# Kernel optimization log

Hardware: AMD Instinct MI355X
Metric: run time of the kernel (lower is better)

## Reference

```python
import jax, jax.numpy as jnp
import numpy as np

B, S, D = 1, 2048, 4096
H, KVH, HD = 32, 8, 128
WIN = 2048
REPEATS = H // KVH
SCALE = HD ** -0.5
NEG = -1e9


def setup_inputs() -> dict:
    key = jax.random.key(0)
    ks = jax.random.split(key, 5)
    x = jax.random.normal(ks[0], (B, S, D), dtype=jnp.float32) * 0.02
    wq = jax.random.normal(ks[1], (H * HD, D), dtype=jnp.float32) * (D ** -0.5)
    wk = jax.random.normal(ks[2], (KVH * HD, D), dtype=jnp.float32) * (D ** -0.5)
    wv = jax.random.normal(ks[3], (KVH * HD, D), dtype=jnp.float32) * (D ** -0.5)
    wo = jax.random.normal(ks[4], (H * HD, D), dtype=jnp.float32).T * ((H * HD) ** -0.5)
    wo = jnp.asarray(wo)  # [D, H*HD] torch-style (out, in) = (D, H*HD)
    positions = jnp.arange(S, dtype=jnp.int32)
    # rotary tables: freqs_cis[s, j] = exp(i * s * theta_j), theta_j = 10000^(-2j/HD)
    theta = 10000.0 ** (-jnp.arange(0, HD, 2, dtype=jnp.float32) / HD)  # [HD/2]
    ang = positions[:, None].astype(jnp.float32) * theta[None, :]       # [S, HD/2]
    freqs_cos = jnp.cos(ang)
    freqs_sin = jnp.sin(ang)
    # sliding-window causal additive mask [S, S]
    i = jnp.arange(S)[:, None]
    j = jnp.arange(S)[None, :]
    allowed = (j <= i) & (i - j < WIN)
    mask = jnp.where(allowed, 0.0, NEG).astype(jnp.float32)
    return {"x": x, "freqs_cos": freqs_cos, "freqs_sin": freqs_sin,
            "wq": wq, "wk": wk, "wv": wv, "wo": wo,
            "mask": mask, "positions": positions}


def _apply_rope(t, cos, sin):
    # t: [B, S, h, HD]; pairs are (even, odd) interleaved -> complex mul
    tr = t[..., 0::2]  # real parts [B,S,h,HD/2]
    ti = t[..., 1::2]  # imag parts
    c = cos[None, :, None, :]
    s = sin[None, :, None, :]
    out_r = tr * c - ti * s
    out_i = tr * s + ti * c
    return jnp.stack([out_r, out_i], axis=-1).reshape(t.shape)


def reference(x, freqs_cos, freqs_sin, wq, wk, wv, wo, mask, positions):
    bsz, seqlen, _ = x.shape
    q = (x @ wq.T).reshape(bsz, seqlen, H, HD)
    k = (x @ wk.T).reshape(bsz, seqlen, KVH, HD)
    v = (x @ wv.T).reshape(bsz, seqlen, KVH, HD)
    q = _apply_rope(q, freqs_cos, freqs_sin)
    k = _apply_rope(k, freqs_cos, freqs_sin)
    # GQA: repeat_interleave kv heads to match query heads (prefill path)
    k = jnp.repeat(k, REPEATS, axis=2)  # [B,S,H,HD]
    v = jnp.repeat(v, REPEATS, axis=2)
    scores = jnp.einsum("bqhd,bkhd->bhqk", q, k) * SCALE
    scores = scores + mask[None, None, :, :]
    probs = jax.nn.softmax(scores, axis=-1)
    out = jnp.einsum("bhqk,bkhd->bqhd", probs, v)
    out = out.reshape(bsz, seqlen, H * HD)
    return out @ wo.T
```

## Files before the change

kernel.cpp:

```cpp
#include <hip/hip_runtime.h>
#include <hip/hip_bf16.h>
#include <stdint.h>

#define SEQ    2048
#define DMODEL 4096
#define NH     32
#define NKVH   8
#define HDIM   128
#define KVD    (NKVH*HDIM)
#define QD     (NH*HDIM)
#define QKVN   (QD + 2*KVD)
#define ASCALE 0.08838834764831845f

typedef __attribute__((ext_vector_type(8))) short s8v;
typedef __attribute__((ext_vector_type(4))) short s4v;
typedef __attribute__((ext_vector_type(4))) float f4v;

#define MFMA16(acc, a, b) \
  asm("v_mfma_f32_16x16x32_bf16 %0, %1, %2, %0" : "+v"(acc) : "v"(a), "v"(b))

#define SBAR() do { __builtin_amdgcn_sched_barrier(0); \
                    __builtin_amdgcn_s_barrier();      \
                    __builtin_amdgcn_sched_barrier(0); } while (0)

__device__ __forceinline__ void gl2lds16(const void* g, void* l) {
  __builtin_amdgcn_global_load_lds(
      (const __attribute__((address_space(1))) void*)g,
      (__attribute__((address_space(3))) void*)l, 16, 0, 0);
}

__global__ __launch_bounds__(256) void k_cvt5(const float* __restrict__ x,
                                              const float* __restrict__ wq,
                                              const float* __restrict__ wk,
                                              const float* __restrict__ wv,
                                              const float* __restrict__ wo,
                                              __hip_bfloat16* __restrict__ xb,
                                              __hip_bfloat16* __restrict__ wf,
                                              __hip_bfloat16* __restrict__ wob) {
  int i = blockIdx.x * 256 + threadIdx.x;
  const float* src;
  __hip_bfloat16* dst;
  float scale = 1.0f;
  if (i < 1048576)       { src = x;  dst = xb; }
  else if (i < 3145728)  { src = wq; dst = wf;  i -= 1048576; scale = ASCALE; }
  else if (i < 3670016)  { src = wk; dst = wf + (size_t)QD * DMODEL;  i -= 3145728; }
  else if (i < 4194304)  { src = wv; dst = wf + (size_t)(QD + KVD) * DMODEL; i -= 3670016; }
  else                   { src = wo; dst = wob; i -= 4194304; }
  const float4* p = (const float4*)src + (size_t)i * 2;
  float4 a = p[0], b = p[1];
  union { __hip_bfloat16 h[8]; s8v v; } o;
  o.h[0] = __float2bfloat16(a.x * scale); o.h[1] = __float2bfloat16(a.y * scale);
  o.h[2] = __float2bfloat16(a.z * scale); o.h[3] = __float2bfloat16(a.w * scale);
  o.h[4] = __float2bfloat16(b.x * scale); o.h[5] = __float2bfloat16(b.y * scale);
  o.h[6] = __float2bfloat16(b.z * scale); o.h[7] = __float2bfloat16(b.w * scale);
  *(s8v*)(dst + (size_t)i * 8) = o.v;
}

__global__ __launch_bounds__(256) void k_rope(__hip_bfloat16* __restrict__ t,
                                              const float* __restrict__ fc,
                                              const float* __restrict__ fs, int heads) {
  int pid = blockIdx.x * 256 + threadIdx.x;
  int i = pid & 63;
  int rest = pid >> 6;
  int h = rest % heads;
  int s = rest / heads;
  size_t base = ((size_t)s * heads + h) * HDIM + 2 * i;
  uint32_t u = *(const uint32_t*)(t + base);
  __hip_bfloat16 hh[2]; *(uint32_t*)hh = u;
  float tr = __bfloat162float(hh[0]), ti = __bfloat162float(hh[1]);
  float c = fc[(size_t)s * 64 + i], sv = fs[(size_t)s * 64 + i];
  hh[0] = __float2bfloat16(tr * c - ti * sv);
  hh[1] = __float2bfloat16(tr * sv + ti * c);
  *(uint32_t*)(t + base) = *(uint32_t*)hh;
}

__global__ __launch_bounds__(512, 2) void k_qkv(const __hip_bfloat16* __restrict__ A,
                                                const __hip_bfloat16* __restrict__ W,
                                                __hip_bfloat16* __restrict__ Qb,
                                                __hip_bfloat16* __restrict__ Kc,
                                                __hip_bfloat16* __restrict__ Vt) {
  __shared__ __align__(16) __hip_bfloat16 sm[2][256 * 64 + 192 * 64];
  const int t5 = threadIdx.x;
  const int wave = t5 >> 6, lane = t5 & 63;
  const int lrow = lane & 15, kq = lane >> 4;
  const int wm = wave >> 1, wn = wave & 1;
  const int mt = blockIdx.x & 7, nt = blockIdx.x >> 3;
  const int m0 = mt * 256, n0 = nt * 192;

  auto stageA = [&](int p, int kt) {
#pragma unroll
    for (int it = 0; it < 4; ++it) {
      int chunk = it * 512 + t5;
      int r = chunk >> 3, cc = ((chunk & 7) ^ (r & 7)) * 8;
      gl2lds16(A + (size_t)(m0 + r) * DMODEL + kt * 64 + cc,
               (char*)&sm[p][0] + it * 8192 + wave * 1024);
    }
  };
  auto stageB = [&](int p, int kt) {
#pragma unroll
    for (int it = 0; it < 3; ++it) {
      int chunk = it * 512 + t5;
      int r = chunk >> 3, cc = ((chunk & 7) ^ (r & 7)) * 8;
      gl2lds16(W + (size_t)(n0 + r) * DMODEL + kt * 64 + cc,
               (char*)&sm[p][0] + 32768 + it * 8192 + wave * 1024);
    }
  };

  f4v acc[4][6] = {};

  stageA(0, 0); stageB(0, 0);
  stageA(1, 1); stageB(1, 1);

  const int NT = DMODEL / 64;
#pragma unroll 2
  for (int t = 0; t < NT; ++t) {
    const int p = t & 1;
    const __hip_bfloat16* As = &sm[p][0];
    const __hip_bfloat16* Bs = &sm[p][256 * 64];

    __builtin_amdgcn_sched_barrier(0);
    if (t == NT - 1) asm volatile("s_waitcnt vmcnt(0)" ::: "memory");
    else             asm volatile("s_waitcnt vmcnt(7)" ::: "memory");
    __builtin_amdgcn_s_barrier();
    __builtin_amdgcn_sched_barrier(0);

    s8v a0[4], b0[6];
#pragma unroll
    for (int m = 0; m < 4; ++m) {
      int row = wm * 64 + m * 16 + lrow;
      a0[m] = *(const s8v*)&As[row * 64 + ((kq * 8) ^ ((row & 7) << 3))];
    }
#pragma unroll
    for (int n = 0; n < 6; ++n) {
      int row = wn * 96 + n * 16 + lrow;
      b0[n] = *(const s8v*)&Bs[row * 64 + ((kq * 8) ^ ((row & 7) << 3))];
    }
    __builtin_amdgcn_s_setprio(1);
#pragma unroll
    for (int m = 0; m < 2; ++m)
#pragma unroll
      for (int n = 0; n < 6; ++n) MFMA16(acc[m][n], a0[m], b0[n]);
    __builtin_amdgcn_s_setprio(0);
    SBAR();

    s8v a1[4], b1[6];
#pragma unroll
    for (int m = 0; m < 4; ++m) {
      int row = wm * 64 + m * 16 + lrow;
      a1[m] = *(const s8v*)&As[row * 64 + ((32 + kq * 8) ^ ((row & 7) << 3))];
    }
#pragma unroll
    for (int n = 0; n < 6; ++n) {
      int row = wn * 96 + n * 16 + lrow;
      b1[n] = *(const s8v*)&Bs[row * 64 + ((32 + kq * 8) ^ ((row & 7) << 3))];
    }
    __builtin_amdgcn_s_setprio(1);
#pragma unroll
    for (int m = 2; m < 4; ++m)
#pragma unroll
      for (int n = 0; n < 6; ++n) MFMA16(acc[m][n], a0[m], b0[n]);
    __builtin_amdgcn_s_setprio(0);
    SBAR();

    if (t + 2 < NT) stageA(p, t + 2);
    __builtin_amdgcn_s_setprio(1);
#pragma unroll
    for (int m = 0; m < 2; ++m)
#pragma unroll
      for (int n = 0; n < 6; ++n) MFMA16(acc[m][n], a1[m], b1[n]);
    __builtin_amdgcn_s_setprio(0);
    SBAR();

    if (t + 2 < NT) stageB(p, t + 2);
    __builtin_amdgcn_s_setprio(1);
#pragma unroll
    for (int m = 2; m < 4; ++m)
#pragma unroll
      for (int n = 0; n < 6; ++n) MFMA16(acc[m][n], a1[m], b1[n]);
    __builtin_amdgcn_s_setprio(0);
  }

#pragma unroll
  for (int m = 0; m < 4; ++m)
#pragma unroll
    for (int n = 0; n < 6; ++n) {
      int c = n0 + wn * 96 + n * 16 + lrow;
      int r0 = m0 + wm * 64 + m * 16 + kq * 4;
      if (c < QD) {
#pragma unroll
        for (int j = 0; j < 4; ++j)
          Qb[(size_t)(r0 + j) * QD + c] = __float2bfloat16(acc[m][n][j]);
      } else if (c < QD + KVD) {
#pragma unroll
        for (int j = 0; j < 4; ++j)
          Kc[(size_t)(r0 + j) * KVD + (c - QD)] = __float2bfloat16(acc[m][n][j]);
      } else {
        union { __hip_bfloat16 b[4]; s4v v; } u;
#pragma unroll
        for (int j = 0; j < 4; ++j) u.b[j] = __float2bfloat16(acc[m][n][j]);
        *(s4v*)&Vt[(size_t)(c - QD - KVD) * SEQ + r0] = u.v;
      }
    }
}

__global__ __launch_bounds__(512, 2) void k_oproj(const __hip_bfloat16* __restrict__ A,
                                                  const __hip_bfloat16* __restrict__ B,
                                                  float* __restrict__ C) {
  __shared__ __align__(16) __hip_bfloat16 sm[2][128 * 64 + 256 * 64];
  const int t5 = threadIdx.x;
  const int wave = t5 >> 6, lane = t5 & 63;
  const int lrow = lane & 15, kq = lane >> 4;
  const int wm = wave >> 2, wn = wave & 3;
  const int m0 = blockIdx.y * 128, n0 = blockIdx.x * 256;

  auto stageA = [&](int p, int kt) {
#pragma unroll
    for (int it = 0; it < 2; ++it) {
      int chunk = it * 512 + t5;
      int r = chunk >> 3, cc = ((chunk & 7) ^ (r & 7)) * 8;
      gl2lds16(A + (size_t)(m0 + r) * QD + kt * 64 + cc,
               (char*)&sm[p][0] + it * 8192 + wave * 1024);
    }
  };
  auto stageB = [&](int p, int kt) {
#pragma unroll
    for (int it = 0; it < 4; ++it) {
      int chunk = it * 512 + t5;
      int r = chunk >> 3, cc = ((chunk & 7) ^ (r & 7)) * 8;
      gl2lds16(B + (size_t)(n0 + r) * QD + kt * 64 + cc,
               (char*)&sm[p][0] + 16384 + it * 8192 + wave * 1024);
    }
  };

  f4v acc[4][4] = {};

  stageA(0, 0); stageB(0, 0);
  stageA(1, 1); stageB(1, 1);

  const int NT = QD / 64;
#pragma unroll 2
  for (int t = 0; t < NT; ++t) {
    const int p = t & 1;
    const __hip_bfloat16* As = &sm[p][0];
    const __hip_bfloat16* Bs = &sm[p][128 * 64];

    __builtin_amdgcn_sched_barrier(0);
    if (t == NT - 1) asm volatile("s_waitcnt vmcnt(0)" ::: "memory");
    else             asm volatile("s_waitcnt vmcnt(6)" ::: "memory");
    __builtin_amdgcn_s_barrier();
    __builtin_amdgcn_sched_barrier(0);

    s8v a0[4], b0[4];
#pragma unroll
    for (int m = 0; m < 4; ++m) {
      int row = wm * 64 + m * 16 + lrow;
      a0[m] = *(const s8v*)&As[row * 64 + ((kq * 8) ^ ((row & 7) << 3))];
    }
#pragma unroll
    for (int n = 0; n < 4; ++n) {
      int row = wn * 64 + n * 16 + lrow;
      b0[n] = *(const s8v*)&Bs[row * 64 + ((kq * 8) ^ ((row & 7) << 3))];
    }
    __builtin_amdgcn_s_setprio(1);
#pragma unroll
    for (int m = 0; m < 2; ++m)
#pragma unroll
      for (int n = 0; n < 4; ++n) MFMA16(acc[m][n], a0[m], b0[n]);
    __builtin_amdgcn_s_setprio(0);
    SBAR();

    s8v a1[4], b1[4];
#pragma unroll
    for (int m = 0; m < 4; ++m) {
      int row = wm * 64 + m * 16 + lrow;
      a1[m] = *(const s8v*)&As[row * 64 + ((32 + kq * 8) ^ ((row & 7) << 3))];
    }
#pragma unroll
    for (int n = 0; n < 4; ++n) {
      int row = wn * 64 + n * 16 + lrow;
      b1[n] = *(const s8v*)&Bs[row * 64 + ((32 + kq * 8) ^ ((row & 7) << 3))];
    }
    __builtin_amdgcn_s_setprio(1);
#pragma unroll
    for (int m = 2; m < 4; ++m)
#pragma unroll
      for (int n = 0; n < 4; ++n) MFMA16(acc[m][n], a0[m], b0[n]);
    __builtin_amdgcn_s_setprio(0);
    SBAR();

    if (t + 2 < NT) stageA(p, t + 2);
    __builtin_amdgcn_s_setprio(1);
#pragma unroll
    for (int m = 0; m < 2; ++m)
#pragma unroll
      for (int n = 0; n < 4; ++n) MFMA16(acc[m][n], a1[m], b1[n]);
    __builtin_amdgcn_s_setprio(0);
    SBAR();

    if (t + 2 < NT) stageB(p, t + 2);
    __builtin_amdgcn_s_setprio(1);
#pragma unroll
    for (int m = 2; m < 4; ++m)
#pragma unroll
      for (int n = 0; n < 4; ++n) MFMA16(acc[m][n], a1[m], b1[n]);
    __builtin_amdgcn_s_setprio(0);
  }

#pragma unroll
  for (int m = 0; m < 4; ++m)
#pragma unroll
    for (int n = 0; n < 4; ++n)
#pragma unroll
      for (int j = 0; j < 4; ++j) {
        int r = m0 + wm * 64 + m * 16 + kq * 4 + j;
        int c = n0 + wn * 64 + n * 16 + lrow;
        C[(size_t)r * DMODEL + c] = acc[m][n][j];
      }
}

__global__ __launch_bounds__(256, 2) void k_flash(const __hip_bfloat16* __restrict__ Q,
                                                  const __hip_bfloat16* __restrict__ Kb,
                                                  const __hip_bfloat16* __restrict__ Vtg,
                                                  __hip_bfloat16* __restrict__ O) {
  __shared__ __align__(16) __hip_bfloat16 Ks[2][64 * 128];
  __shared__ __align__(16) __hip_bfloat16 Vs[128 * 64];
  __shared__ __align__(16) __hip_bfloat16 Ps[4][16 * 64];
  const int qp = blockIdx.x, h = blockIdx.y, g = h >> 2;
  const int t = threadIdx.x, wave = t >> 6, lane = t & 63;
  const int lrow = lane & 15, kq = lane >> 4;
  const int qtA = qp, qtB = 31 - qp;

  s8v qfA[4], qfB[4];
  {
    const int qrA = qtA * 64 + wave * 16 + lrow;
    const int qrB = qtB * 64 + wave * 16 + lrow;
#pragma unroll
    for (int tt = 0; tt < 4; ++tt) {
      qfA[tt] = *(const s8v*)(Q + (size_t)qrA * QD + h * HDIM + tt * 32 + kq * 8);
      qfB[tt] = *(const s8v*)(Q + (size_t)qrB * QD + h * HDIM + tt * 32 + kq * 8);
    }
  }

  f4v oA[8] = {}, oB[8] = {};
  float mA = -1e30f, mB = -1e30f;
  float lA = 0.f, lB = 0.f;

  auto stage_k = [&](int buf, int kv) {
#pragma unroll
    for (int it = 0; it < 4; ++it) {
      int chunk = it * 256 + t;
      int r = chunk >> 4, cc = ((chunk & 15) ^ (r & 7)) * 8;
      gl2lds16(Kb + (size_t)(kv * 64 + r) * KVD + g * HDIM + cc,
               (char*)&Ks[buf][0] + it * 4096 + wave * 1024);
    }
  };
  auto stage_v = [&](int kv) {
#pragma unroll
    for (int it = 0; it < 4; ++it) {
      int chunk = it * 256 + t;
      int d = chunk >> 3, cc = ((chunk & 7) ^ (d & 7)) * 8;
      gl2lds16(Vtg + (size_t)(g * HDIM + d) * SEQ + kv * 64 + cc,
               (char*)Vs + it * 4096 + wave * 1024);
    }
  };

  auto soft_pv = [&](f4v (&s)[4], int qt, int kv, f4v (&acc_o)[8], float& mrun, float& lrun) {
    __hip_bfloat16* P = &Ps[wave][0];
    const bool diag = (kv == qt);
    const int qi = qt * 64 + wave * 16 + lrow;
    const int swz = (lrow & 7) << 3;
    float pv[4][4];
    float mx = -1e30f;
#pragma unroll
    for (int n = 0; n < 4; ++n)
#pragma unroll
      for (int j = 0; j < 4; ++j) {
        float v = s[n][j];
        if (diag) {
          int ki = kv * 64 + n * 16 + kq * 4 + j;
          if (ki > qi) v = -1e30f;
        }
        pv[n][j] = v;
        mx = fmaxf(mx, v);
      }
    mx = fmaxf(mx, __shfl_xor(mx, 16, 64));
    mx = fmaxf(mx, __shfl_xor(mx, 32, 64));
    if (!__all(mx <= mrun)) {
      float mnew = fmaxf(mrun, mx);
      float fsc = __expf(mrun - mnew);
      mrun = mnew;
      lrun *= fsc;
      float fj[4];
#pragma unroll
      for (int j = 0; j < 4; ++j) fj[j] = __shfl(fsc, kq * 4 + j, 64);
#pragma unroll
      for (int n = 0; n < 8; ++n) {
        acc_o[n][0] *= fj[0]; acc_o[n][1] *= fj[1];
        acc_o[n][2] *= fj[2]; acc_o[n][3] *= fj[3];
      }
    }
    float rsum = 0.f;
    asm volatile("" ::: "memory");
#pragma unroll
    for (int n = 0; n < 4; ++n) {
      union { __hip_bfloat16 b[4]; s4v v; } u;
#pragma unroll
      for (int j = 0; j < 4; ++j) {
        __hip_bfloat16 pb = __float2bfloat16(__expf(pv[n][j] - mrun));
        u.b[j] = pb;
        rsum += __bfloat162float(pb);
      }
      *(s4v*)&P[lrow * 64 + ((n * 16 + kq * 4) ^ swz)] = u.v;
    }
    rsum += __shfl_xor(rsum, 16, 64);
    rsum += __shfl_xor(rsum, 32, 64);
    lrun += rsum;
    asm volatile("" ::: "memory");
#pragma unroll
    for (int tt = 0; tt < 2; ++tt) {
      s8v pa = *(const s8v*)&P[lrow * 64 + ((tt * 32 + kq * 8) ^ swz)];
#pragma unroll
      for (int n = 0; n < 8; ++n) {
        int d = n * 16 + lrow;
        s8v vf = *(const s8v*)&Vs[d * 64 + ((tt * 32 + kq * 8) ^ ((d & 7) << 3))];
        MFMA16(acc_o[n], pa, vf);
      }
    }
  };

  stage_k(0, 0);
  int cur = 0;
  for (int kv = 0; kv <= qtB; ++kv) {
    const bool actA = (kv <= qtA);
    __syncthreads();
    if (kv < qtB) stage_k(cur ^ 1, kv + 1);
    stage_v(kv);

    f4v sB[4] = {}, sA[4] = {};
    if (actA) {
#pragma unroll
      for (int tt = 0; tt < 4; ++tt)
#pragma unroll
        for (int n = 0; n < 4; ++n) {
          int row = n * 16 + lrow;
          s8v kf = *(const s8v*)&Ks[cur][row * 128 + ((tt * 32 + kq * 8) ^ ((row & 7) << 3))];
          MFMA16(sB[n], kf, qfB[tt]);
          MFMA16(sA[n], kf, qfA[tt]);
        }
    } else {
#pragma unroll
      for (int tt = 0; tt < 4; ++tt)
#pragma unroll
        for (int n = 0; n < 4; ++n) {
          int row = n * 16 + lrow;
          s8v kf = *(const s8v*)&Ks[cur][row * 128 + ((tt * 32 + kq * 8) ^ ((row & 7) << 3))];
          MFMA16(sB[n], kf, qfB[tt]);
        }
    }
    __syncthreads();

    soft_pv(sB, qtB, kv, oB, mB, lB);
    if (actA) soft_pv(sA, qtA, kv, oA, mA, lA);
    cur ^= 1;
  }

  float ljB[4], ljA[4];
#pragma unroll
  for (int j = 0; j < 4; ++j) {
    ljB[j] = __shfl(lB, kq * 4 + j, 64);
    ljA[j] = __shfl(lA, kq * 4 + j, 64);
  }
#pragma unroll
  for (int n = 0; n < 8; ++n)
#pragma unroll
    for (int j = 0; j < 4; ++j) {
      int d = n * 16 + lrow;
      int qiB = qtB * 64 + wave * 16 + kq * 4 + j;
      O[(size_t)qiB * QD + h * HDIM + d] = __float2bfloat16(oB[n][j] / ljB[j]);
      int qiA = qtA * 64 + wave * 16 + kq * 4 + j;
      O[(size_t)qiA * QD + h * HDIM + d] = __float2bfloat16(oA[n][j] / ljA[j]);
    }
}

extern "C" void kernel_launch(void* const* d_in, const int* in_sizes, int n_in,
                              void* d_out, int out_size, void* d_ws, size_t ws_size,
                              hipStream_t stream) {
  const float* x  = (const float*)d_in[0];
  const float* fc = (const float*)d_in[1];
  const float* fs = (const float*)d_in[2];
  const float* wq = (const float*)d_in[3];
  const float* wk = (const float*)d_in[4];
  const float* wv = (const float*)d_in[5];
  const float* wo = (const float*)d_in[6];
  float* out = (float*)d_out;

  char* ws = (char*)d_ws;
  auto alloc = [&](size_t bytes) {
    char* p = ws;
    ws += (bytes + 255) & ~(size_t)255;
    return p;
  };
  __hip_bfloat16* xb  = (__hip_bfloat16*)alloc((size_t)SEQ * DMODEL * 2);
  __hip_bfloat16* wf  = (__hip_bfloat16*)alloc((size_t)QKVN * DMODEL * 2);
  __hip_bfloat16* wob = (__hip_bfloat16*)alloc((size_t)DMODEL * QD * 2);
  __hip_bfloat16* Qb  = (__hip_bfloat16*)alloc((size_t)SEQ * QD * 2);
  __hip_bfloat16* Kc  = (__hip_bfloat16*)alloc((size_t)SEQ * KVD * 2);
  __hip_bfloat16* Vtg = (__hip_bfloat16*)alloc((size_t)KVD * SEQ * 2);
  __hip_bfloat16* Ob  = (__hip_bfloat16*)alloc((size_t)SEQ * QD * 2);

  k_cvt5<<<dim3(24576), dim3(256), 0, stream>>>(x, wq, wk, wv, wo, xb, wf, wob);

  k_qkv<<<dim3(256), dim3(512), 0, stream>>>(xb, wf, Qb, Kc, Vtg);

  k_rope<<<dim3(SEQ * NH * 64 / 256), 256, 0, stream>>>(Qb, fc, fs, NH);
  k_rope<<<dim3(SEQ * NKVH * 64 / 256), 256, 0, stream>>>(Kc, fc, fs, NKVH);

  k_flash<<<dim3(16, NH), 256, 0, stream>>>(Qb, Kc, Vtg, Ob);

  k_oproj<<<dim3(DMODEL / 256, SEQ / 128), dim3(512), 0, stream>>>(Ob, wob, out);
}
```

Before: 280.5 us.

## Fuse RoPE into QKV GEMM epilogue and compute softmax row sums via MFMA

RoPE is now applied inside the QKV projection epilogue, using a lane shuffle to fetch each element's rotary partner. This drops two separate rope kernels and their read-modify-write passes over Q and K. In flash attention, the running softmax denominator is no longer built from scalar adds and shuffles. Instead an extra block of ones is appended to the V tile in LDS, so a ninth MFMA column accumulates the row sum. This adds MFMA work and accumulator registers, and the epilogue does extra uncoalesced cos/sin loads.

```diff
diff --git a/kernel.cpp b/kernel.cpp
--- a/kernel.cpp
+++ b/kernel.cpp
@@ -56,26 +56,10 @@
   *(s8v*)(dst + (size_t)i * 8) = o.v;
 }
 
-__global__ __launch_bounds__(256) void k_rope(__hip_bfloat16* __restrict__ t,
-                                              const float* __restrict__ fc,
-                                              const float* __restrict__ fs, int heads) {
-  int pid = blockIdx.x * 256 + threadIdx.x;
-  int i = pid & 63;
-  int rest = pid >> 6;
-  int h = rest % heads;
-  int s = rest / heads;
-  size_t base = ((size_t)s * heads + h) * HDIM + 2 * i;
-  uint32_t u = *(const uint32_t*)(t + base);
-  __hip_bfloat16 hh[2]; *(uint32_t*)hh = u;
-  float tr = __bfloat162float(hh[0]), ti = __bfloat162float(hh[1]);
-  float c = fc[(size_t)s * 64 + i], sv = fs[(size_t)s * 64 + i];
-  hh[0] = __float2bfloat16(tr * c - ti * sv);
-  hh[1] = __float2bfloat16(tr * sv + ti * c);
-  *(uint32_t*)(t + base) = *(uint32_t*)hh;
-}
-
 __global__ __launch_bounds__(512, 2) void k_qkv(const __hip_bfloat16* __restrict__ A,
                                                 const __hip_bfloat16* __restrict__ W,
+                                                const float* __restrict__ fc,
+                                                const float* __restrict__ fs,
                                                 __hip_bfloat16* __restrict__ Qb,
                                                 __hip_bfloat16* __restrict__ Kc,
                                                 __hip_bfloat16* __restrict__ Vt) {
@@ -186,14 +170,27 @@
     for (int n = 0; n < 6; ++n) {
       int c = n0 + wn * 96 + n * 16 + lrow;
       int r0 = m0 + wm * 64 + m * 16 + kq * 4;
-      if (c < QD) {
-#pragma unroll
-        for (int j = 0; j < 4; ++j)
-          Qb[(size_t)(r0 + j) * QD + c] = __float2bfloat16(acc[m][n][j]);
-      } else if (c < QD + KVD) {
-#pragma unroll
-        for (int j = 0; j < 4; ++j)
-          Kc[(size_t)(r0 + j) * KVD + (c - QD)] = __float2bfloat16(acc[m][n][j]);
+      if (c < QD + KVD) {
+        const int ii = (c & 127) >> 1;
+        const bool odd = c & 1;
+        float vout[4];
+#pragma unroll
+        for (int j = 0; j < 4; ++j) {
+          float v = acc[m][n][j];
+          float pvt = __shfl_xor(v, 1, 64);
+          float cv = fc[(size_t)(r0 + j) * 64 + ii];
+          float sv = fs[(size_t)(r0 + j) * 64 + ii];
+          vout[j] = odd ? (pvt * sv + v * cv) : (v * cv - pvt * sv);
+        }
+        if (c < QD) {
+#pragma unroll
+          for (int j = 0; j < 4; ++j)
+            Qb[(size_t)(r0 + j) * QD + c] = __float2bfloat16(vout[j]);
+        } else {
+#pragma unroll
+          for (int j = 0; j < 4; ++j)
+            Kc[(size_t)(r0 + j) * KVD + (c - QD)] = __float2bfloat16(vout[j]);
+        }
       } else {
         union { __hip_bfloat16 b[4]; s4v v; } u;
 #pragma unroll
@@ -323,7 +320,7 @@
                                                   const __hip_bfloat16* __restrict__ Vtg,
                                                   __hip_bfloat16* __restrict__ O) {
   __shared__ __align__(16) __hip_bfloat16 Ks[2][64 * 128];
-  __shared__ __align__(16) __hip_bfloat16 Vs[128 * 64];
+  __shared__ __align__(16) __hip_bfloat16 Vs[144 * 64];
   __shared__ __align__(16) __hip_bfloat16 Ps[4][16 * 64];
   const int qp = blockIdx.x, h = blockIdx.y, g = h >> 2;
   const int t = threadIdx.x, wave = t >> 6, lane = t & 63;
@@ -341,9 +338,15 @@
     }
   }
 
-  f4v oA[8] = {}, oB[8] = {};
+  if (t < 128) {
+    union { __hip_bfloat16 h8[8]; s8v v; } one;
+#pragma unroll
+    for (int e = 0; e < 8; ++e) one.h8[e] = __float2bfloat16(1.0f);
+    *(s8v*)&Vs[128 * 64 + t * 8] = one.v;
+  }
+
+  f4v oA[9] = {}, oB[9] = {};
   float mA = -1e30f, mB = -1e30f;
-  float lA = 0.f, lB = 0.f;
 
   auto stage_k = [&](int buf, int kv) {
 #pragma unroll
@@ -364,7 +367,7 @@
     }
   };
 
-  auto soft_pv = [&](f4v (&s)[4], int qt, int kv, f4v (&acc_o)[8], float& mrun, float& lrun) {
+  auto soft_pv = [&](f4v (&s)[4], int qt, int kv, f4v (&acc_o)[9], float& mrun) {
     __hip_bfloat16* P = &Ps[wave][0];
     const bool diag = (kv == qt);
     const int qi = qt * 64 + wave * 16 + lrow;
@@ -389,38 +392,29 @@
       float mnew = fmaxf(mrun, mx);
       float fsc = __expf(mrun - mnew);
       mrun = mnew;
-      lrun *= fsc;
       float fj[4];
 #pragma unroll
       for (int j = 0; j < 4; ++j) fj[j] = __shfl(fsc, kq * 4 + j, 64);
 #pragma unroll
-      for (int n = 0; n < 8; ++n) {
+      for (int n = 0; n < 9; ++n) {
         acc_o[n][0] *= fj[0]; acc_o[n][1] *= fj[1];
         acc_o[n][2] *= fj[2]; acc_o[n][3] *= fj[3];
       }
     }
-    float rsum = 0.f;
     asm volatile("" ::: "memory");
 #pragma unroll
     for (int n = 0; n < 4; ++n) {
       union { __hip_bfloat16 b[4]; s4v v; } u;
 #pragma unroll
-      for (int j = 0; j < 4; ++j) {
-        __hip_bfloat16 pb = __float2bfloat16(__expf(pv[n][j] - mrun));
-        u.b[j] = pb;
-        rsum += __bfloat162float(pb);
-      }
+      for (int j = 0; j < 4; ++j) u.b[j] = __float2bfloat16(__expf(pv[n][j] - mrun));
       *(s4v*)&P[lrow * 64 + ((n * 16 + kq * 4) ^ swz)] = u.v;
     }
-    rsum += __shfl_xor(rsum, 16, 64);
-    rsum += __shfl_xor(rsum, 32, 64);
-    lrun += rsum;
     asm volatile("" ::: "memory");
 #pragma unroll
     for (int tt = 0; tt < 2; ++tt) {
       s8v pa = *(const s8v*)&P[lrow * 64 + ((tt * 32 + kq * 8) ^ swz)];
 #pragma unroll
-      for (int n = 0; n < 8; ++n) {
+      for (int n = 0; n < 9; ++n) {
         int d = n * 16 + lrow;
         s8v vf = *(const s8v*)&Vs[d * 64 + ((tt * 32 + kq * 8) ^ ((d & 7) << 3))];
         MFMA16(acc_o[n], pa, vf);
@@ -459,26 +453,20 @@
     }
     __syncthreads();
 
-    soft_pv(sB, qtB, kv, oB, mB, lB);
-    if (actA) soft_pv(sA, qtA, kv, oA, mA, lA);
+    soft_pv(sB, qtB, kv, oB, mB);
+    if (actA) soft_pv(sA, qtA, kv, oA, mA);
     cur ^= 1;
   }
 
-  float ljB[4], ljA[4];
-#pragma unroll
-  for (int j = 0; j < 4; ++j) {
-    ljB[j] = __shfl(lB, kq * 4 + j, 64);
-    ljA[j] = __shfl(lA, kq * 4 + j, 64);
-  }
 #pragma unroll
   for (int n = 0; n < 8; ++n)
 #pragma unroll
     for (int j = 0; j < 4; ++j) {
       int d = n * 16 + lrow;
       int qiB = qtB * 64 + wave * 16 + kq * 4 + j;
-      O[(size_t)qiB * QD + h * HDIM + d] = __float2bfloat16(oB[n][j] / ljB[j]);
+      O[(size_t)qiB * QD + h * HDIM + d] = __float2bfloat16(oB[n][j] / oB[8][j]);
       int qiA = qtA * 64 + wave * 16 + kq * 4 + j;
-      O[(size_t)qiA * QD + h * HDIM + d] = __float2bfloat16(oA[n][j] / ljA[j]);
+      O[(size_t)qiA * QD + h * HDIM + d] = __float2bfloat16(oA[n][j] / oA[8][j]);
     }
 }
 
@@ -510,10 +498,7 @@
 
   k_cvt5<<<dim3(24576), dim3(256), 0, stream>>>(x, wq, wk, wv, wo, xb, wf, wob);
 
-  k_qkv<<<dim3(256), dim3(512), 0, stream>>>(xb, wf, Qb, Kc, Vtg);
-
-  k_rope<<<dim3(SEQ * NH * 64 / 256), 256, 0, stream>>>(Qb, fc, fs, NH);
-  k_rope<<<dim3(SEQ * NKVH * 64 / 256), 256, 0, stream>>>(Kc, fc, fs, NKVH);
+  k_qkv<<<dim3(256), dim3(512), 0, stream>>>(xb, wf, fc, fs, Qb, Kc, Vtg);
 
   k_flash<<<dim3(16, NH), 256, 0, stream>>>(Qb, Kc, Vtg, Ob);
 
```

Result: faster. 267.1 us (-4.8%).
